# Optimization experiments

Hardware: AMD Instinct MI355X
Metric: run time of the kernel (lower is better)

The kernel has to match this reference:

```python
import jax, jax.numpy as jnp
import numpy as np

B, N, XD = 4, 8192, 256   # batch, seq len, input/kv feature dim
F, H = 512, 8             # features, heads
D = F // H                # per-head dim = 64
EPS = 1e-6                # flax LayerNorm default epsilon


def _layer_norm(t, scale, bias):
    mu = jnp.mean(t, axis=-1, keepdims=True)
    var = jnp.mean(jnp.square(t - mu), axis=-1, keepdims=True)
    return (t - mu) * jax.lax.rsqrt(var + EPS) * scale + bias


def setup_inputs() -> dict:
    key = jax.random.key(0)
    ks = jax.random.split(key, 5)
    return {
        "x": jax.random.normal(ks[0], (B, N, XD), jnp.float32),
        "kv": jax.random.normal(ks[1], (B, N, XD), jnp.float32),
        # linen.initializers.normal(1/x_dim) / normal(1/h_dim)
        "Q": jax.random.normal(ks[2], (XD, F), jnp.float32) * (1.0 / XD),
        "K": jax.random.normal(ks[3], (XD, F), jnp.float32) * (1.0 / XD),
        "V": jax.random.normal(ks[4], (XD, F), jnp.float32) * (1.0 / XD),
        "log_scale": jnp.zeros((F,), jnp.float32),
        "ln_q_scale": jnp.ones((D,), jnp.float32),
        "ln_q_bias": jnp.zeros((D,), jnp.float32),
        "ln_k_scale": jnp.ones((D,), jnp.float32),
        "ln_k_bias": jnp.zeros((D,), jnp.float32),
        "ln_v_scale": jnp.ones((D,), jnp.float32),
        "ln_v_bias": jnp.zeros((D,), jnp.float32),
    }


def reference(x, kv, Q, K, V, log_scale,
              ln_q_scale, ln_q_bias, ln_k_scale, ln_k_bias, ln_v_scale, ln_v_bias):
    # QKV projections (value scaled by exp(log_scale) per feature)
    query = x @ Q                                    # [B, N, F]
    key = kv @ K                                     # [B, N, F]
    value = jnp.exp(log_scale) * (kv @ V)            # [B, N, F]
    # reshape exactly as the source module does
    q = query.reshape(B, H, -1, D)                   # [B, H, N, D]
    k = key.reshape(B, H, -1, D)
    v = value.reshape(B, H, -1, D)
    # per-head LayerNorm over the head dim (layer_norm=True)
    q = _layer_norm(q, ln_q_scale, ln_q_bias)
    k = _layer_norm(k, ln_k_scale, ln_k_bias)
    v = _layer_norm(v, ln_v_scale, ln_v_bias)
    # galerkin linear attention: Q @ (K^T V) / seq_len, no softmax, no NxN scores
    seq_len = k.shape[-2]
    ctx = jnp.einsum('bhnd,bhne->bhde', k, v)        # [B, H, D, D]
    out = jnp.einsum('bhnd,bhde->bhne', q, ctx) / seq_len
    return out.reshape(B, N, F)
```

## Files before the change

kernel.cpp:

```cpp
#include <hip/hip_runtime.h>
#include <stdint.h>

using f32x4  = __attribute__((ext_vector_type(4))) float;
using short8 = __attribute__((ext_vector_type(8))) short;
using u16x4  = __attribute__((ext_vector_type(4))) unsigned short;

#define MFMA(a, b, c) __builtin_amdgcn_mfma_f32_16x16x32_bf16((a), (b), (c), 0, 0, 0)

#define XDIM 256
#define FDIM 512
#define EPS  1e-6f

#define QT_OFF    0u
#define KT_OFF    262144u
#define VT_OFF    524288u
#define CTXT_OFF  786432u
#define PART_OFF  1048576u

static __device__ __forceinline__ unsigned short f2bf(float f) {
  unsigned u = __float_as_uint(f);
  unsigned r = u + 0x7FFFu + ((u >> 16) & 1u);
  return (unsigned short)(r >> 16);
}

static __device__ __forceinline__ void stage_a_full(const float* a_rows, int tid, char* Alds) {
  const int r = tid >> 2, cq = tid & 3;
  const float* src = a_rows + (size_t)r * XDIM + cq * 64;
  char* dst = Alds + r * 528 + cq * 128;
#pragma unroll
  for (int i = 0; i < 4; ++i) {
    float4 f0 = *(const float4*)(src + i * 16);
    float4 f1 = *(const float4*)(src + i * 16 + 4);
    float4 f2 = *(const float4*)(src + i * 16 + 8);
    float4 f3 = *(const float4*)(src + i * 16 + 12);
    short8 v0, v1;
    v0[0] = (short)f2bf(f0.x); v0[1] = (short)f2bf(f0.y);
    v0[2] = (short)f2bf(f0.z); v0[3] = (short)f2bf(f0.w);
    v0[4] = (short)f2bf(f1.x); v0[5] = (short)f2bf(f1.y);
    v0[6] = (short)f2bf(f1.z); v0[7] = (short)f2bf(f1.w);
    v1[0] = (short)f2bf(f2.x); v1[1] = (short)f2bf(f2.y);
    v1[2] = (short)f2bf(f2.z); v1[3] = (short)f2bf(f2.w);
    v1[4] = (short)f2bf(f3.x); v1[5] = (short)f2bf(f3.y);
    v1[6] = (short)f2bf(f3.z); v1[7] = (short)f2bf(f3.w);
    *(short8*)(dst + i * 32)      = v0;
    *(short8*)(dst + i * 32 + 16) = v1;
  }
}

static __device__ __forceinline__ void chunk_layernorm(f32x4 acc[4][4], const float* sc,
                                                       const float* bs, int lane) {
  const int lr = lane & 15;
  float scl[4], bia[4];
#pragma unroll
  for (int nt = 0; nt < 4; ++nt) { scl[nt] = sc[nt * 16 + lr]; bia[nt] = bs[nt * 16 + lr]; }
#pragma unroll
  for (int mt = 0; mt < 4; ++mt) {
#pragma unroll
    for (int j = 0; j < 4; ++j) {
      float a0 = acc[mt][0][j], a1 = acc[mt][1][j], a2 = acc[mt][2][j], a3 = acc[mt][3][j];
      float s  = a0 + a1 + a2 + a3;
      float s2 = a0 * a0 + a1 * a1 + a2 * a2 + a3 * a3;
#pragma unroll
      for (int off = 1; off < 16; off <<= 1) {
        s  += __shfl_xor(s, off, 16);
        s2 += __shfl_xor(s2, off, 16);
      }
      const float mu  = s * (1.0f / 64.0f);
      const float var = s2 * (1.0f / 64.0f) - mu * mu;
      const float rs  = rsqrtf(var + EPS);
#pragma unroll
      for (int nt = 0; nt < 4; ++nt)
        acc[mt][nt][j] = (acc[mt][nt][j] - mu) * rs * scl[nt] + bia[nt];
    }
  }
}

__global__ void prep_weights_kernel(const float* __restrict__ Q, const float* __restrict__ K,
                                    const float* __restrict__ V, const float* __restrict__ ls,
                                    unsigned short* __restrict__ Qt, unsigned short* __restrict__ Kt,
                                    unsigned short* __restrict__ Vt) {
  const int flat = blockIdx.x * 256 + threadIdx.x;
  const int mat = flat >> 17;
  const int rem = flat & 131071;
  const int f = rem & 511;
  const int k = rem >> 9;
  if (mat == 0)      Qt[f * 256 + k] = f2bf(Q[k * 512 + f]);
  else if (mat == 1) Kt[f * 256 + k] = f2bf(K[k * 512 + f]);
  else               Vt[f * 256 + k] = f2bf(V[k * 512 + f] * expf(ls[f]));
}

__launch_bounds__(256, 2)
__global__ void kv_ctx_kernel(const float* __restrict__ kv,
                              const unsigned short* __restrict__ Kt,
                              const unsigned short* __restrict__ Vt,
                              const float* __restrict__ lnk_s, const float* __restrict__ lnk_b,
                              const float* __restrict__ lnv_s, const float* __restrict__ lnv_b,
                              float* __restrict__ partials) {
  __shared__ __align__(16) char smem[33792];

  const int tid = threadIdx.x, lane = tid & 63, w = tid >> 6;
  const int bid = blockIdx.x, rb = bid >> 1, nb = bid & 1;
  const int row0 = rb * 64;
  const int lr = lane & 15, lk = lane >> 4;
  const int koff = lk * 16;

  stage_a_full(kv + (size_t)row0 * XDIM, tid, smem);

  const f32x4 z4 = {0.f, 0.f, 0.f, 0.f};
  f32x4 acck[4][4], accv[4][4];
#pragma unroll
  for (int i = 0; i < 4; ++i)
#pragma unroll
    for (int j = 0; j < 4; ++j) { acck[i][j] = z4; accv[i][j] = z4; }

  const char* kbase = (const char*)Kt + (size_t)(nb * 256 + w * 64) * 512;
  const char* vbase = (const char*)Vt + (size_t)(nb * 256 + w * 64) * 512;

  __syncthreads();

#pragma unroll
  for (int ks = 0; ks < 4; ++ks) {
    short8 a0[4], a1[4];
#pragma unroll
    for (int mt = 0; mt < 4; ++mt) {
      const char* ar = smem + (mt * 16 + lr) * 528 + ks * 128;
      a0[mt] = *(const short8*)(ar + koff);
      a1[mt] = *(const short8*)(ar + 64 + koff);
    }
    {
      short8 b0[4], b1[4];
#pragma unroll
      for (int nt = 0; nt < 4; ++nt) {
        const char* kr = kbase + (size_t)(nt * 16 + lr) * 512 + ks * 128 + koff;
        b0[nt] = *(const short8*)(kr);
        b1[nt] = *(const short8*)(kr + 64);
      }
#pragma unroll
      for (int mt = 0; mt < 4; ++mt)
#pragma unroll
        for (int nt = 0; nt < 4; ++nt) {
          acck[mt][nt] = MFMA(a0[mt], b0[nt], acck[mt][nt]);
          acck[mt][nt] = MFMA(a1[mt], b1[nt], acck[mt][nt]);
        }
    }
    {
      short8 b0[4], b1[4];
#pragma unroll
      for (int nt = 0; nt < 4; ++nt) {
        const char* vr = vbase + (size_t)(nt * 16 + lr) * 512 + ks * 128 + koff;
        b0[nt] = *(const short8*)(vr);
        b1[nt] = *(const short8*)(vr + 64);
      }
#pragma unroll
      for (int mt = 0; mt < 4; ++mt)
#pragma unroll
        for (int nt = 0; nt < 4; ++nt) {
          accv[mt][nt] = MFMA(a0[mt], b0[nt], accv[mt][nt]);
          accv[mt][nt] = MFMA(a1[mt], b1[nt], accv[mt][nt]);
        }
    }
  }

  chunk_layernorm(acck, lnk_s, lnk_b, lane);
  chunk_layernorm(accv, lnv_s, lnv_b, lane);

  char* knT = smem;
  char* vnT = smem + 16384;
  f32x4 cacc[4];
#pragma unroll
  for (int i = 0; i < 4; ++i) cacc[i] = z4;
  const int drow = w * 16 + lr;

#pragma unroll
  for (int half = 0; half < 2; ++half) {
    __syncthreads();
    if ((w >> 1) == half) {
      const int tb2 = (w & 1) * 128;
#pragma unroll
      for (int mt = 0; mt < 4; ++mt) {
        const int tb = tb2 + mt * 32 + lk * 8;
#pragma unroll
        for (int nt = 0; nt < 4; ++nt) {
          const int d = nt * 16 + lr;
          u16x4 pk, pv;
#pragma unroll
          for (int j = 0; j < 4; ++j) {
            pk[j] = f2bf(acck[mt][nt][j]);
            pv[j] = f2bf(accv[mt][nt][j]);
          }
          const int boff = d * 256 + (tb ^ ((d & 7) << 4));
          *(u16x4*)(knT + boff) = pk;
          *(u16x4*)(vnT + boff) = pv;
        }
      }
    }
    __syncthreads();
#pragma unroll
    for (int s = 0; s < 4; ++s) {
      const short8 a = *(const short8*)(knT + drow * 256 + ((s * 64 + koff) ^ ((drow & 7) << 4)));
#pragma unroll
      for (int nt = 0; nt < 4; ++nt) {
        const int e = nt * 16 + lr;
        const short8 b = *(const short8*)(vnT + e * 256 + ((s * 64 + koff) ^ ((e & 7) << 4)));
        cacc[nt] = MFMA(a, b, cacc[nt]);
      }
    }
  }

  float* pout = partials + (size_t)bid * 4096;
#pragma unroll
  for (int nt = 0; nt < 4; ++nt)
#pragma unroll
    for (int j = 0; j < 4; ++j)
      pout[(w * 16 + lk * 4 + j) * 64 + nt * 16 + lr] = cacc[nt][j];
}

__global__ void reduce_ctx_kernel(const float* __restrict__ partials,
                                  unsigned short* __restrict__ ctxTg) {
  const int bid = blockIdx.x, t = threadIdx.x;
  const int gg = bid >> 3, sl = bid & 7;
  const float* base = partials + (size_t)gg * 32 * 4096;
#pragma unroll
  for (int rep = 0; rep < 2; ++rep) {
    const int idx = sl * 512 + rep * 256 + t;
    float acc = 0.f;
#pragma unroll 8
    for (int p = 0; p < 32; ++p) acc += base[(size_t)p * 4096 + idx];
    const int d = idx >> 6, e = idx & 63;
    ctxTg[(size_t)gg * 4096 + e * 64 + d] = f2bf(acc * (1.0f / 8192.0f));
  }
}

__launch_bounds__(256, 2)
__global__ void q_out_kernel(const float* __restrict__ x, const unsigned short* __restrict__ Qt,
                             const unsigned short* __restrict__ ctxTg,
                             const float* __restrict__ lnq_s, const float* __restrict__ lnq_b,
                             float* __restrict__ out) {
  __shared__ __align__(16) char smem[43008];

  const int tid = threadIdx.x, lane = tid & 63, w = tid >> 6;
  const int bid = blockIdx.x, rb = bid >> 1, nb = bid & 1;
  const int row0 = rb * 64;
  const int g = row0 >> 10;
  const int lr = lane & 15, lk = lane >> 4;
  const int koff = lk * 16;
  char* ctxT = smem + 33792;

  stage_a_full(x + (size_t)row0 * XDIM, tid, smem);

  {
    const unsigned short* src = ctxTg + (size_t)g * 4096 + (tid >> 2) * 64 + (tid & 3) * 16;
    char* dst = ctxT + (tid >> 2) * 144 + (tid & 3) * 32;
    *(short8*)dst        = *(const short8*)(src);
    *(short8*)(dst + 16) = *(const short8*)(src + 8);
  }

  const f32x4 z4 = {0.f, 0.f, 0.f, 0.f};
  f32x4 acc[4][4];
#pragma unroll
  for (int i = 0; i < 4; ++i)
#pragma unroll
    for (int j = 0; j < 4; ++j) acc[i][j] = z4;

  const char* qbase = (const char*)Qt + (size_t)(nb * 256 + w * 64) * 512;

  __syncthreads();

#pragma unroll
  for (int ks = 0; ks < 4; ++ks) {
    short8 a0[4], a1[4], b0[4], b1[4];
#pragma unroll
    for (int mt = 0; mt < 4; ++mt) {
      const char* ar = smem + (mt * 16 + lr) * 528 + ks * 128;
      a0[mt] = *(const short8*)(ar + koff);
      a1[mt] = *(const short8*)(ar + 64 + koff);
    }
#pragma unroll
    for (int nt = 0; nt < 4; ++nt) {
      const char* qr = qbase + (size_t)(nt * 16 + lr) * 512 + ks * 128 + koff;
      b0[nt] = *(const short8*)(qr);
      b1[nt] = *(const short8*)(qr + 64);
    }
#pragma unroll
    for (int mt = 0; mt < 4; ++mt)
#pragma unroll
      for (int nt = 0; nt < 4; ++nt) {
        acc[mt][nt] = MFMA(a0[mt], b0[nt], acc[mt][nt]);
        acc[mt][nt] = MFMA(a1[mt], b1[nt], acc[mt][nt]);
      }
  }

  chunk_layernorm(acc, lnq_s, lnq_b, lane);

  __syncthreads();

  char* A2 = smem + w * 8192;
#pragma unroll
  for (int mt = 0; mt < 4; ++mt)
#pragma unroll
    for (int j = 0; j < 4; ++j) {
      const int m = mt * 16 + lk * 4 + j;
      const int sw = (m & 7) << 4;
#pragma unroll
      for (int nt = 0; nt < 4; ++nt) {
        const int d = nt * 16 + lr;
        *(unsigned short*)(A2 + m * 128 + ((d * 2) ^ sw)) = f2bf(acc[mt][nt][j]);
      }
    }
  __syncthreads();

  f32x4 o[4][4];
#pragma unroll
  for (int i = 0; i < 4; ++i)
#pragma unroll
    for (int j = 0; j < 4; ++j) o[i][j] = z4;

#pragma unroll
  for (int s = 0; s < 2; ++s) {
    short8 a[4], b[4];
#pragma unroll
    for (int mt = 0; mt < 4; ++mt) {
      const int m = mt * 16 + lr;
      a[mt] = *(const short8*)(A2 + m * 128 + ((s * 64 + koff) ^ ((m & 7) << 4)));
    }
#pragma unroll
    for (int nt = 0; nt < 4; ++nt)
      b[nt] = *(const short8*)(ctxT + (nt * 16 + lr) * 144 + s * 64 + koff);
#pragma unroll
    for (int mt = 0; mt < 4; ++mt)
#pragma unroll
      for (int nt = 0; nt < 4; ++nt)
        o[mt][nt] = MFMA(a[mt], b[nt], o[mt][nt]);
  }

#pragma unroll
  for (int mt = 0; mt < 4; ++mt)
#pragma unroll
    for (int nt = 0; nt < 4; ++nt)
#pragma unroll
      for (int j = 0; j < 4; ++j) {
        const int n = mt * 16 + lk * 4 + j;
        out[(size_t)(row0 + n) * FDIM + nb * 256 + w * 64 + nt * 16 + lr] = o[mt][nt][j];
      }
}

extern "C" void kernel_launch(void* const* d_in, const int* in_sizes, int n_in,
                              void* d_out, int out_size, void* d_ws, size_t ws_size,
                              hipStream_t stream) {
  (void)in_sizes; (void)n_in; (void)out_size; (void)ws_size;
  const float* x     = (const float*)d_in[0];
  const float* kv    = (const float*)d_in[1];
  const float* Q     = (const float*)d_in[2];
  const float* K     = (const float*)d_in[3];
  const float* V     = (const float*)d_in[4];
  const float* ls    = (const float*)d_in[5];
  const float* lnq_s = (const float*)d_in[6];
  const float* lnq_b = (const float*)d_in[7];
  const float* lnk_s = (const float*)d_in[8];
  const float* lnk_b = (const float*)d_in[9];
  const float* lnv_s = (const float*)d_in[10];
  const float* lnv_b = (const float*)d_in[11];
  float* out = (float*)d_out;

  char* ws = (char*)d_ws;
  unsigned short* Qt   = (unsigned short*)(ws + QT_OFF);
  unsigned short* Kt   = (unsigned short*)(ws + KT_OFF);
  unsigned short* Vt   = (unsigned short*)(ws + VT_OFF);
  unsigned short* ctxT = (unsigned short*)(ws + CTXT_OFF);
  float* partials      = (float*)(ws + PART_OFF);

  prep_weights_kernel<<<1536, 256, 0, stream>>>(Q, K, V, ls, Qt, Kt, Vt);
  kv_ctx_kernel<<<1024, 256, 0, stream>>>(kv, Kt, Vt, lnk_s, lnk_b, lnv_s, lnv_b, partials);
  reduce_ctx_kernel<<<256, 256, 0, stream>>>(partials, ctxT);
  q_out_kernel<<<1024, 256, 0, stream>>>(x, Qt, ctxT, lnq_s, lnq_b, out);
}
```

Baseline: 125.9 us.

## Split KV projection and context into separate kernels via global bf16 intermediates

The fused kv/context kernel becomes two kernels. A projection kernel computes K or V per block, with no LDS, and writes layer-normed bf16 transposed tiles to global memory. A context kernel then reads them back to form the per-group partial K^T V. The 1/N scale and transpose move from the reduce kernel into q_out, which also gains register double-buffering of Qt loads and a remapped block order. This aims to raise occupancy and drop the in-block LDS round-trips, but it adds roughly 64 MB of extra global traffic and one more launch.

```diff
diff --git a/kernel.cpp b/kernel.cpp
--- a/kernel.cpp
+++ b/kernel.cpp
@@ -14,8 +14,10 @@
 #define QT_OFF    0u
 #define KT_OFF    262144u
 #define VT_OFF    524288u
-#define CTXT_OFF  786432u
-#define PART_OFF  1048576u
+#define CTX_OFF   786432u
+#define KNT_OFF   1310720u
+#define VNT_OFF   34865152u
+#define PART_OFF  68419584u
 
 static __device__ __forceinline__ unsigned short f2bf(float f) {
   unsigned u = __float_as_uint(f);
@@ -23,28 +25,15 @@
   return (unsigned short)(r >> 16);
 }
 
-static __device__ __forceinline__ void stage_a_full(const float* a_rows, int tid, char* Alds) {
-  const int r = tid >> 2, cq = tid & 3;
-  const float* src = a_rows + (size_t)r * XDIM + cq * 64;
-  char* dst = Alds + r * 528 + cq * 128;
-#pragma unroll
-  for (int i = 0; i < 4; ++i) {
-    float4 f0 = *(const float4*)(src + i * 16);
-    float4 f1 = *(const float4*)(src + i * 16 + 4);
-    float4 f2 = *(const float4*)(src + i * 16 + 8);
-    float4 f3 = *(const float4*)(src + i * 16 + 12);
-    short8 v0, v1;
-    v0[0] = (short)f2bf(f0.x); v0[1] = (short)f2bf(f0.y);
-    v0[2] = (short)f2bf(f0.z); v0[3] = (short)f2bf(f0.w);
-    v0[4] = (short)f2bf(f1.x); v0[5] = (short)f2bf(f1.y);
-    v0[6] = (short)f2bf(f1.z); v0[7] = (short)f2bf(f1.w);
-    v1[0] = (short)f2bf(f2.x); v1[1] = (short)f2bf(f2.y);
-    v1[2] = (short)f2bf(f2.z); v1[3] = (short)f2bf(f2.w);
-    v1[4] = (short)f2bf(f3.x); v1[5] = (short)f2bf(f3.y);
-    v1[6] = (short)f2bf(f3.z); v1[7] = (short)f2bf(f3.w);
-    *(short8*)(dst + i * 32)      = v0;
-    *(short8*)(dst + i * 32 + 16) = v1;
-  }
+static __device__ __forceinline__ short8 load8_f32_bf16(const float* p) {
+  float4 f0 = *(const float4*)(p);
+  float4 f1 = *(const float4*)(p + 4);
+  short8 v;
+  v[0] = (short)f2bf(f0.x); v[1] = (short)f2bf(f0.y);
+  v[2] = (short)f2bf(f0.z); v[3] = (short)f2bf(f0.w);
+  v[4] = (short)f2bf(f1.x); v[5] = (short)f2bf(f1.y);
+  v[6] = (short)f2bf(f1.z); v[7] = (short)f2bf(f1.w);
+  return v;
 }
 
 static __device__ __forceinline__ void chunk_layernorm(f32x4 acc[4][4], const float* sc,
@@ -89,121 +78,98 @@
   else               Vt[f * 256 + k] = f2bf(V[k * 512 + f] * expf(ls[f]));
 }
 
-__launch_bounds__(256, 2)
-__global__ void kv_ctx_kernel(const float* __restrict__ kv,
-                              const unsigned short* __restrict__ Kt,
-                              const unsigned short* __restrict__ Vt,
-                              const float* __restrict__ lnk_s, const float* __restrict__ lnk_b,
-                              const float* __restrict__ lnv_s, const float* __restrict__ lnv_b,
-                              float* __restrict__ partials) {
-  __shared__ __align__(16) char smem[33792];
-
+__launch_bounds__(256, 3)
+__global__ void proj_kernel(const float* __restrict__ kv,
+                            const unsigned short* __restrict__ Kt,
+                            const unsigned short* __restrict__ Vt,
+                            const float* __restrict__ lnk_s, const float* __restrict__ lnk_b,
+                            const float* __restrict__ lnv_s, const float* __restrict__ lnv_b,
+                            unsigned short* __restrict__ knT, unsigned short* __restrict__ vnT) {
   const int tid = threadIdx.x, lane = tid & 63, w = tid >> 6;
-  const int bid = blockIdx.x, rb = bid >> 1, nb = bid & 1;
+  const int bid = blockIdx.x;
+  const int rb = bid >> 2;
+  const int mat = (bid >> 1) & 1;
+  const int nb = bid & 1;
   const int row0 = rb * 64;
+  const int g = rb >> 4;
   const int lr = lane & 15, lk = lane >> 4;
-  const int koff = lk * 16;
-
-  stage_a_full(kv + (size_t)row0 * XDIM, tid, smem);
 
   const f32x4 z4 = {0.f, 0.f, 0.f, 0.f};
-  f32x4 acck[4][4], accv[4][4];
+  f32x4 acc[4][4];
 #pragma unroll
   for (int i = 0; i < 4; ++i)
 #pragma unroll
-    for (int j = 0; j < 4; ++j) { acck[i][j] = z4; accv[i][j] = z4; }
-
-  const char* kbase = (const char*)Kt + (size_t)(nb * 256 + w * 64) * 512;
-  const char* vbase = (const char*)Vt + (size_t)(nb * 256 + w * 64) * 512;
-
-  __syncthreads();
+    for (int j = 0; j < 4; ++j) acc[i][j] = z4;
+
+  const unsigned short* wt = mat ? Vt : Kt;
+  const char* bbase = (const char*)(wt + (size_t)(nb * 256 + w * 64) * 256);
 
 #pragma unroll
   for (int ks = 0; ks < 4; ++ks) {
-    short8 a0[4], a1[4];
+    short8 a0[4], a1[4], b0[4], b1[4];
 #pragma unroll
     for (int mt = 0; mt < 4; ++mt) {
-      const char* ar = smem + (mt * 16 + lr) * 528 + ks * 128;
-      a0[mt] = *(const short8*)(ar + koff);
-      a1[mt] = *(const short8*)(ar + 64 + koff);
-    }
-    {
-      short8 b0[4], b1[4];
+      const float* ar = kv + (size_t)(row0 + mt * 16 + lr) * XDIM + ks * 64 + lk * 8;
+      a0[mt] = load8_f32_bf16(ar);
+      a1[mt] = load8_f32_bf16(ar + 32);
+    }
+#pragma unroll
+    for (int nt = 0; nt < 4; ++nt) {
+      const char* br = bbase + (size_t)(nt * 16 + lr) * 512 + ks * 128 + lk * 16;
+      b0[nt] = *(const short8*)(br);
+      b1[nt] = *(const short8*)(br + 64);
+    }
+#pragma unroll
+    for (int mt = 0; mt < 4; ++mt)
 #pragma unroll
       for (int nt = 0; nt < 4; ++nt) {
-        const char* kr = kbase + (size_t)(nt * 16 + lr) * 512 + ks * 128 + koff;
-        b0[nt] = *(const short8*)(kr);
-        b1[nt] = *(const short8*)(kr + 64);
-      }
-#pragma unroll
-      for (int mt = 0; mt < 4; ++mt)
-#pragma unroll
-        for (int nt = 0; nt < 4; ++nt) {
-          acck[mt][nt] = MFMA(a0[mt], b0[nt], acck[mt][nt]);
-          acck[mt][nt] = MFMA(a1[mt], b1[nt], acck[mt][nt]);
-        }
-    }
-    {
-      short8 b0[4], b1[4];
-#pragma unroll
-      for (int nt = 0; nt < 4; ++nt) {
-        const char* vr = vbase + (size_t)(nt * 16 + lr) * 512 + ks * 128 + koff;
-        b0[nt] = *(const short8*)(vr);
-        b1[nt] = *(const short8*)(vr + 64);
-      }
-#pragma unroll
-      for (int mt = 0; mt < 4; ++mt)
-#pragma unroll
-        for (int nt = 0; nt < 4; ++nt) {
-          accv[mt][nt] = MFMA(a0[mt], b0[nt], accv[mt][nt]);
-          accv[mt][nt] = MFMA(a1[mt], b1[nt], accv[mt][nt]);
-        }
-    }
-  }
-
-  chunk_layernorm(acck, lnk_s, lnk_b, lane);
-  chunk_layernorm(accv, lnv_s, lnv_b, lane);
-
-  char* knT = smem;
-  char* vnT = smem + 16384;
+        acc[mt][nt] = MFMA(a0[mt], b0[nt], acc[mt][nt]);
+        acc[mt][nt] = MFMA(a1[mt], b1[nt], acc[mt][nt]);
+      }
+  }
+
+  chunk_layernorm(acc, mat ? lnv_s : lnk_s, mat ? lnv_b : lnk_b, lane);
+
+  unsigned short* dst = mat ? vnT : knT;
+  const int c = nb * 4 + w;
+  const int tbase = c * 1024 + (rb & 15) * 64;
+#pragma unroll
+  for (int mt = 0; mt < 4; ++mt)
+#pragma unroll
+    for (int nt = 0; nt < 4; ++nt) {
+      const int d = nt * 16 + lr;
+      u16x4 p;
+#pragma unroll
+      for (int j = 0; j < 4; ++j) p[j] = f2bf(acc[mt][nt][j]);
+      *(u16x4*)(dst + (size_t)(g * 64 + d) * 8192 + tbase + mt * 16 + lk * 4) = p;
+    }
+}
+
+__launch_bounds__(256, 4)
+__global__ void ctx_kernel(const unsigned short* __restrict__ knT,
+                           const unsigned short* __restrict__ vnT,
+                           float* __restrict__ partials) {
+  const int tid = threadIdx.x, lane = tid & 63, w = tid >> 6;
+  const int bid = blockIdx.x;
+  const int g = bid >> 5, sp = bid & 31;
+  const int lr = lane & 15, lk = lane >> 4;
+
+  const f32x4 z4 = {0.f, 0.f, 0.f, 0.f};
   f32x4 cacc[4];
 #pragma unroll
   for (int i = 0; i < 4; ++i) cacc[i] = z4;
-  const int drow = w * 16 + lr;
-
-#pragma unroll
-  for (int half = 0; half < 2; ++half) {
-    __syncthreads();
-    if ((w >> 1) == half) {
-      const int tb2 = (w & 1) * 128;
-#pragma unroll
-      for (int mt = 0; mt < 4; ++mt) {
-        const int tb = tb2 + mt * 32 + lk * 8;
-#pragma unroll
-        for (int nt = 0; nt < 4; ++nt) {
-          const int d = nt * 16 + lr;
-          u16x4 pk, pv;
-#pragma unroll
-          for (int j = 0; j < 4; ++j) {
-            pk[j] = f2bf(acck[mt][nt][j]);
-            pv[j] = f2bf(accv[mt][nt][j]);
-          }
-          const int boff = d * 256 + (tb ^ ((d & 7) << 4));
-          *(u16x4*)(knT + boff) = pk;
-          *(u16x4*)(vnT + boff) = pv;
-        }
-      }
-    }
-    __syncthreads();
-#pragma unroll
-    for (int s = 0; s < 4; ++s) {
-      const short8 a = *(const short8*)(knT + drow * 256 + ((s * 64 + koff) ^ ((drow & 7) << 4)));
-#pragma unroll
-      for (int nt = 0; nt < 4; ++nt) {
-        const int e = nt * 16 + lr;
-        const short8 b = *(const short8*)(vnT + e * 256 + ((s * 64 + koff) ^ ((e & 7) << 4)));
-        cacc[nt] = MFMA(a, b, cacc[nt]);
-      }
+
+  const int d = w * 16 + lr;
+  const unsigned short* abase = knT + (size_t)(g * 64 + d) * 8192 + sp * 256 + lk * 8;
+  const unsigned short* bbase = vnT + (size_t)(g * 64) * 8192 + sp * 256 + lk * 8;
+
+#pragma unroll
+  for (int ksi = 0; ksi < 8; ++ksi) {
+    const short8 a = *(const short8*)(abase + ksi * 32);
+#pragma unroll
+    for (int nt = 0; nt < 4; ++nt) {
+      const short8 b = *(const short8*)(bbase + (size_t)(nt * 16 + lr) * 8192 + ksi * 32);
+      cacc[nt] = MFMA(a, b, cacc[nt]);
     }
   }
 
@@ -216,7 +182,7 @@
 }
 
 __global__ void reduce_ctx_kernel(const float* __restrict__ partials,
-                                  unsigned short* __restrict__ ctxTg) {
+                                  float* __restrict__ ctxf) {
   const int bid = blockIdx.x, t = threadIdx.x;
   const int gg = bid >> 3, sl = bid & 7;
   const float* base = partials + (size_t)gg * 32 * 4096;
@@ -226,33 +192,48 @@
     float acc = 0.f;
 #pragma unroll 8
     for (int p = 0; p < 32; ++p) acc += base[(size_t)p * 4096 + idx];
-    const int d = idx >> 6, e = idx & 63;
-    ctxTg[(size_t)gg * 4096 + e * 64 + d] = f2bf(acc * (1.0f / 8192.0f));
+    ctxf[(size_t)gg * 4096 + idx] = acc;
   }
 }
 
 __launch_bounds__(256, 2)
 __global__ void q_out_kernel(const float* __restrict__ x, const unsigned short* __restrict__ Qt,
-                             const unsigned short* __restrict__ ctxTg,
+                             const float* __restrict__ ctx,
                              const float* __restrict__ lnq_s, const float* __restrict__ lnq_b,
                              float* __restrict__ out) {
   __shared__ __align__(16) char smem[43008];
 
   const int tid = threadIdx.x, lane = tid & 63, w = tid >> 6;
-  const int bid = blockIdx.x, rb = bid >> 1, nb = bid & 1;
+  const int bid = blockIdx.x;
+  const int rb = ((bid >> 4) << 3) | (bid & 7);
+  const int nb = (bid >> 3) & 1;
   const int row0 = rb * 64;
   const int g = row0 >> 10;
   const int lr = lane & 15, lk = lane >> 4;
   const int koff = lk * 16;
   char* ctxT = smem + 33792;
 
-  stage_a_full(x + (size_t)row0 * XDIM, tid, smem);
-
   {
-    const unsigned short* src = ctxTg + (size_t)g * 4096 + (tid >> 2) * 64 + (tid & 3) * 16;
-    char* dst = ctxT + (tid >> 2) * 144 + (tid & 3) * 32;
-    *(short8*)dst        = *(const short8*)(src);
-    *(short8*)(dst + 16) = *(const short8*)(src + 8);
+    const int r = tid >> 2, cq = tid & 3;
+    const float* src = x + (size_t)(row0 + r) * XDIM + cq * 64;
+    char* dst = smem + r * 528 + cq * 128;
+#pragma unroll
+    for (int i = 0; i < 4; ++i) {
+      short8 v0 = load8_f32_bf16(src + i * 16);
+      short8 v1 = load8_f32_bf16(src + i * 16 + 8);
+      *(short8*)(dst + i * 32)      = v0;
+      *(short8*)(dst + i * 32 + 16) = v1;
+    }
+  }
+
+  {
+    const int d = tid >> 2, e0 = (tid & 3) * 16;
+    const float* csrc = ctx + (size_t)g * 4096 + d * 64 + e0;
+#pragma unroll
+    for (int i = 0; i < 16; ++i) {
+      const unsigned short v = f2bf(csrc[i] * (1.0f / 8192.0f));
+      *(unsigned short*)(ctxT + (e0 + i) * 144 + d * 2) = v;
+    }
   }
 
   const f32x4 z4 = {0.f, 0.f, 0.f, 0.f};
@@ -264,29 +245,41 @@
 
   const char* qbase = (const char*)Qt + (size_t)(nb * 256 + w * 64) * 512;
 
+  short8 buf0[8], buf1[8];
+#pragma unroll
+  for (int nt = 0; nt < 4; ++nt) {
+    const char* r = qbase + (size_t)(nt * 16 + lr) * 512 + koff;
+    buf0[nt * 2]     = *(const short8*)(r);
+    buf0[nt * 2 + 1] = *(const short8*)(r + 64);
+  }
+
   __syncthreads();
 
 #pragma unroll
   for (int ks = 0; ks < 4; ++ks) {
-    short8 a0[4], a1[4], b0[4], b1[4];
+    if (ks < 3) {
+      short8* nxt = ((ks & 1) == 0) ? buf1 : buf0;
+#pragma unroll
+      for (int nt = 0; nt < 4; ++nt) {
+        const char* r = qbase + (size_t)(nt * 16 + lr) * 512 + (ks + 1) * 128 + koff;
+        nxt[nt * 2]     = *(const short8*)(r);
+        nxt[nt * 2 + 1] = *(const short8*)(r + 64);
+      }
+    }
+    short8 a0[4], a1[4];
 #pragma unroll
     for (int mt = 0; mt < 4; ++mt) {
       const char* ar = smem + (mt * 16 + lr) * 528 + ks * 128;
       a0[mt] = *(const short8*)(ar + koff);
       a1[mt] = *(const short8*)(ar + 64 + koff);
     }
-#pragma unroll
-    for (int nt = 0; nt < 4; ++nt) {
-      const char* qr = qbase + (size_t)(nt * 16 + lr) * 512 + ks * 128 + koff;
-      b0[nt] = *(const short8*)(qr);
-      b1[nt] = *(const short8*)(qr + 64);
-    }
+    const short8* cur = ((ks & 1) == 0) ? buf0 : buf1;
 #pragma unroll
     for (int mt = 0; mt < 4; ++mt)
 #pragma unroll
       for (int nt = 0; nt < 4; ++nt) {
-        acc[mt][nt] = MFMA(a0[mt], b0[nt], acc[mt][nt]);
-        acc[mt][nt] = MFMA(a1[mt], b1[nt], acc[mt][nt]);
+        acc[mt][nt] = MFMA(a0[mt], cur[nt * 2],     acc[mt][nt]);
+        acc[mt][nt] = MFMA(a1[mt], cur[nt * 2 + 1], acc[mt][nt]);
       }
   }
 
@@ -363,14 +356,17 @@
   float* out = (float*)d_out;
 
   char* ws = (char*)d_ws;
-  unsigned short* Qt   = (unsigned short*)(ws + QT_OFF);
-  unsigned short* Kt   = (unsigned short*)(ws + KT_OFF);
-  unsigned short* Vt   = (unsigned short*)(ws + VT_OFF);
-  unsigned short* ctxT = (unsigned short*)(ws + CTXT_OFF);
-  float* partials      = (float*)(ws + PART_OFF);
+  unsigned short* Qt  = (unsigned short*)(ws + QT_OFF);
+  unsigned short* Kt  = (unsigned short*)(ws + KT_OFF);
+  unsigned short* Vt  = (unsigned short*)(ws + VT_OFF);
+  float* ctx          = (float*)(ws + CTX_OFF);
+  unsigned short* knT = (unsigned short*)(ws + KNT_OFF);
+  unsigned short* vnT = (unsigned short*)(ws + VNT_OFF);
+  float* partials     = (float*)(ws + PART_OFF);
 
   prep_weights_kernel<<<1536, 256, 0, stream>>>(Q, K, V, ls, Qt, Kt, Vt);
-  kv_ctx_kernel<<<1024, 256, 0, stream>>>(kv, Kt, Vt, lnk_s, lnk_b, lnv_s, lnv_b, partials);
-  reduce_ctx_kernel<<<256, 256, 0, stream>>>(partials, ctxT);
-  q_out_kernel<<<1024, 256, 0, stream>>>(x, Qt, ctxT, lnq_s, lnq_b, out);
-}
+  proj_kernel<<<2048, 256, 0, stream>>>(kv, Kt, Vt, lnk_s, lnk_b, lnv_s, lnv_b, knT, vnT);
+  ctx_kernel<<<1024, 256, 0, stream>>>(knT, vnT, partials);
+  reduce_ctx_kernel<<<256, 256, 0, stream>>>(partials, ctx);
+  q_out_kernel<<<1024, 256, 0, stream>>>(x, Qt, ctx, lnq_s, lnq_b, out);
+}
```

Measured after the change: 174.4 us. +38.6%, slower.
